# Performance work log

Hardware: AMD Instinct MI355X
Metric: run time of the kernel (lower is better)

The kernel has to match this reference:

```python
import jax, jax.numpy as jnp
import numpy as np

N_NODES = 50000
IN_C = 128
OUT_C = 128
N_EDGES = 1600000
NEG_SLOPE = 0.2
EPS = 1e-16  # matches torch_geometric softmax denominator epsilon


def setup_inputs() -> dict:
    key = jax.random.key(0)
    k1, k2, k3, k4, k5 = jax.random.split(key, 5)
    glorot = 1.0 / np.sqrt(IN_C)
    x = jax.random.normal(k1, (N_NODES, IN_C), dtype=jnp.float32)
    W = jax.random.normal(k2, (IN_C, OUT_C), dtype=jnp.float32) * glorot
    a_src = jax.random.normal(k3, (OUT_C,), dtype=jnp.float32) * glorot
    a_dst = jax.random.normal(k4, (OUT_C,), dtype=jnp.float32) * glorot
    bias = jnp.zeros((OUT_C,), dtype=jnp.float32)
    edge_index = jax.random.randint(k5, (2, N_EDGES), 0, N_NODES, dtype=jnp.int32)
    return {"x": x, "W": W, "a_src": a_src, "a_dst": a_dst,
            "bias": bias, "edge_index": edge_index}


def reference(x, W, a_src, a_dst, bias, edge_index):
    N = x.shape[0]
    # add self loops (GATConv default add_self_loops=True)
    loops = jnp.arange(N, dtype=edge_index.dtype)
    src = jnp.concatenate([edge_index[0], loops])  # [E+N]
    dst = jnp.concatenate([edge_index[1], loops])

    h = x @ W                                      # [N, out]
    alpha_s = h @ a_src                            # [N]
    alpha_d = h @ a_dst                            # [N]

    e = alpha_s[src] + alpha_d[dst]                # [E+N]
    e = jnp.where(e > 0, e, NEG_SLOPE * e)         # leaky_relu

    # neighbor-wise (per destination node) stable softmax
    m = jax.ops.segment_max(e, dst, num_segments=N)
    ex = jnp.exp(e - m[dst])
    denom = jax.ops.segment_sum(ex, dst, num_segments=N)
    alpha = ex / (denom[dst] + EPS)

    # weighted aggregation of source features into destination nodes
    msgs = h[src] * alpha[:, None]                 # [E+N, out]
    out = jax.ops.segment_sum(msgs, dst, num_segments=N) + bias
    return jax.nn.relu(out)
```

## Files before the change

### kernel.cpp

```cpp
#include <hip/hip_runtime.h>
#include <hip/hip_fp16.h>

#define C 128
#define NEG_SLOPE 0.2f
#define SM_EPS 1e-16f
#define BKT_SHIFT 8
#define BKT_MASK 255
#define GB_CHUNK 2048
#define WP 136

typedef unsigned int uint32;
typedef __attribute__((ext_vector_type(8))) short bf16x8;
typedef __attribute__((ext_vector_type(4))) float f32x4;

static __device__ __forceinline__ unsigned short f2bf(float f) {
    uint32 u = __float_as_uint(f);
    uint32 r = 0x7FFFu + ((u >> 16) & 1u);
    return (unsigned short)((u + r) >> 16);
}
static __device__ __forceinline__ uint32 f2bf2(float lo, float hi) {
    return (uint32)f2bf(lo) | ((uint32)f2bf(hi) << 16);
}
static __device__ __forceinline__ uint32 f2h(float f) {
    __half h = __float2half(f);
    return (uint32)*reinterpret_cast<unsigned short*>(&h);
}
static __device__ __forceinline__ float h2f(uint32 b) {
    unsigned short s = (unsigned short)(b & 0xffffu);
    __half h = *reinterpret_cast<__half*>(&s);
    return __half2float(h);
}

__global__ __launch_bounds__(256) void cvtw_hist_kernel(
    const float* __restrict__ W, uint32* __restrict__ Wf,
    const int* __restrict__ dst, int* __restrict__ bucket_cnt,
    int E, int total, int NB)
{
    __shared__ int bhist[256];
    const int tid = threadIdx.x;
    bhist[tid] = 0;
    const int gid = blockIdx.x * 256 + tid;
    if (gid < 8192) {
        int j2   = gid & 3;
        int lane = (gid >> 2) & 63;
        int tile = gid >> 8;
        int t = tile >> 2, kk = tile & 3;
        int n = t * 16 + (lane & 15);
        int k = kk * 32 + (lane >> 4) * 8 + j2 * 2;
        Wf[gid] = f2bf2(W[k * C + n], W[(k + 1) * C + n]);
    }
    __syncthreads();
    const int stride = gridDim.x * 256;
    for (int i = gid; i < total; i += stride) {
        int d = (i < E) ? dst[i] : (i - E);
        atomicAdd(&bhist[d >> BKT_SHIFT], 1);
    }
    __syncthreads();
    if (tid < NB && bhist[tid]) atomicAdd(&bucket_cnt[tid], bhist[tid]);
}

__global__ __launch_bounds__(256) void gemm_bin_kernel(
    const float* __restrict__ x, const uint32* __restrict__ Wf,
    const float* __restrict__ a_src, const float* __restrict__ a_dst,
    unsigned short* __restrict__ hb, float* __restrict__ as_out,
    float* __restrict__ ad_out, int N,
    const int* __restrict__ src, const int* __restrict__ dst,
    const int* __restrict__ bucket_cnt, int* __restrict__ bucket_progress,
    uint32* __restrict__ packed, int E, int total, int NB)
{
    __shared__ __align__(16) unsigned short slice[4][16 * WP];
    __shared__ int hist[256];
    __shared__ int base[256];
    __shared__ int boff[256];
    __shared__ int wave_tot[4];

    const int tid  = threadIdx.x;
    const int lane = tid & 63;
    const int w    = tid >> 6;
    const int row0 = blockIdx.x * 64;
    const int m16  = lane & 15;
    const int q    = lane >> 4;

    if (row0 < N) {
        const int row = row0 + w * 16 + m16;
        const bool rv = (row < N);
        const float* xr_p = x + (size_t)(rv ? row : 0) * C + q * 8;

        float4 xr[8];
        #pragma unroll
        for (int kk = 0; kk < 4; ++kk) {
            xr[kk * 2]     = rv ? *(const float4*)(xr_p + kk * 32)     : make_float4(0, 0, 0, 0);
            xr[kk * 2 + 1] = rv ? *(const float4*)(xr_p + kk * 32 + 4) : make_float4(0, 0, 0, 0);
        }

        f32x4 acc[8];
        const f32x4 zz = {0.f, 0.f, 0.f, 0.f};
        #pragma unroll
        for (int t = 0; t < 8; ++t) acc[t] = zz;

        #pragma unroll
        for (int kk = 0; kk < 4; ++kk) {
            union { bf16x8 v; uint32 u[4]; } au;
            float4 p0 = xr[kk * 2], p1 = xr[kk * 2 + 1];
            au.u[0] = f2bf2(p0.x, p0.y); au.u[1] = f2bf2(p0.z, p0.w);
            au.u[2] = f2bf2(p1.x, p1.y); au.u[3] = f2bf2(p1.z, p1.w);
            #pragma unroll
            for (int t = 0; t < 8; ++t) {
                bf16x8 b = *(const bf16x8*)&Wf[((t * 4 + kk) * 64 + lane) * 4];
                acc[t] = __builtin_amdgcn_mfma_f32_16x16x32_bf16(au.v, b, acc[t], 0, 0, 0);
            }
        }

        float ps[4] = {0.f, 0.f, 0.f, 0.f}, pd[4] = {0.f, 0.f, 0.f, 0.f};
        #pragma unroll
        for (int t = 0; t < 8; ++t) {
            float av = a_src[t * 16 + m16];
            float dv = a_dst[t * 16 + m16];
            #pragma unroll
            for (int r = 0; r < 4; ++r) {
                ps[r] += acc[t][r] * av;
                pd[r] += acc[t][r] * dv;
            }
        }
        #pragma unroll
        for (int r = 0; r < 4; ++r) {
            #pragma unroll
            for (int off = 1; off < 16; off <<= 1) {
                ps[r] += __shfl_xor(ps[r], off, 64);
                pd[r] += __shfl_xor(pd[r], off, 64);
            }
        }
        if (m16 == 0) {
            #pragma unroll
            for (int r = 0; r < 4; ++r) {
                int rr = row0 + w * 16 + q * 4 + r;
                if (rr < N) { as_out[rr] = ps[r]; ad_out[rr] = pd[r]; }
            }
        }

        #pragma unroll
        for (int t = 0; t < 8; ++t)
            #pragma unroll
            for (int r = 0; r < 4; ++r)
                slice[w][(q * 4 + r) * WP + t * 16 + m16] = f2bf(acc[t][r]);
        __syncthreads();
        #pragma unroll
        for (int it = 0; it < 4; ++it) {
            int r = it * 4 + q;
            int rr = row0 + w * 16 + r;
            if (rr < N) {
                bf16x8 v = *(const bf16x8*)&slice[w][r * WP + m16 * 8];
                *(bf16x8*)&hb[(size_t)rr * C + m16 * 8] = v;
            }
        }
    }

    const int start = blockIdx.x * GB_CHUNK;
    if (start >= total) return;
    const int end = min(start + GB_CHUNK, total);

    hist[tid] = 0;
    int v = (tid < NB) ? bucket_cnt[tid] : 0;
    int xx = v;
    #pragma unroll
    for (int o = 1; o < 64; o <<= 1) {
        int t = __shfl_up(xx, o, 64);
        if (lane >= o) xx += t;
    }
    if (lane == 63) wave_tot[w] = xx;
    __syncthreads();
    {
        int wbase = 0;
        #pragma unroll
        for (int w2 = 0; w2 < 4; ++w2) wbase += (w2 < w) ? wave_tot[w2] : 0;
        boff[tid] = wbase + xx - v;
    }

    int es[8], ed[8];
    #pragma unroll
    for (int k = 0; k < 8; ++k) {
        int i = start + k * 256 + tid;
        if (i < end) {
            es[k] = (i < E) ? src[i] : (i - E);
            ed[k] = (i < E) ? dst[i] : (i - E);
        } else ed[k] = -1;
    }
    #pragma unroll
    for (int k = 0; k < 8; ++k)
        if (ed[k] >= 0) atomicAdd(&hist[ed[k] >> BKT_SHIFT], 1);
    __syncthreads();
    if (tid < NB) {
        int c = hist[tid];
        base[tid] = boff[tid] + (c ? atomicAdd(&bucket_progress[tid], c) : 0);
    }
    hist[tid] = 0;
    __syncthreads();
    #pragma unroll
    for (int k = 0; k < 8; ++k) {
        if (ed[k] >= 0) {
            int b = ed[k] >> BKT_SHIFT;
            int pos = base[b] + atomicAdd(&hist[b], 1);
            packed[pos] = ((uint32)es[k] << BKT_SHIFT) | (uint32)(ed[k] & BKT_MASK);
        }
    }
}

__global__ __launch_bounds__(1024) void build_kernel(
    const uint32* __restrict__ packed, const int* __restrict__ bucket_cnt,
    const float* __restrict__ as, const float* __restrict__ ad,
    int* __restrict__ row_start, uint32* __restrict__ csr, int N, int NB, int total)
{
    __shared__ int cnt[256];
    __shared__ int cur[256];
    __shared__ float adl[256];
    __shared__ int boff[256];
    __shared__ int wave_tot[8];
    const int tid = threadIdx.x;
    const int b = blockIdx.x;

    int v = 0, xx = 0;
    if (tid < 256) {
        const int lane = tid & 63;
        v = (tid < NB) ? bucket_cnt[tid] : 0;
        xx = v;
        #pragma unroll
        for (int o = 1; o < 64; o <<= 1) {
            int t = __shfl_up(xx, o, 64);
            if (lane >= o) xx += t;
        }
        if (lane == 63) wave_tot[tid >> 6] = xx;
        cnt[tid] = 0;
        int g = (b << BKT_SHIFT) + tid;
        adl[tid] = (g < N) ? ad[g] : 0.f;
    }
    __syncthreads();
    if (tid < 256) {
        const int wid = tid >> 6;
        int wbase = 0;
        #pragma unroll
        for (int w = 0; w < 4; ++w) wbase += (w < wid) ? wave_tot[w] : 0;
        boff[tid] = wbase + xx - v;
    }
    __syncthreads();
    const int off = boff[b];
    const int end = off + ((b < NB) ? bucket_cnt[b] : 0);
    if (b == 0 && tid == 0) row_start[N] = total;

    for (int j = off + tid; j < end; j += 1024)
        atomicAdd(&cnt[packed[j] & BKT_MASK], 1);
    __syncthreads();

    int v2 = 0, x2 = 0;
    if (tid < 256) {
        const int lane = tid & 63;
        v2 = cnt[tid]; x2 = v2;
        #pragma unroll
        for (int o = 1; o < 64; o <<= 1) {
            int t = __shfl_up(x2, o, 64);
            if (lane >= o) x2 += t;
        }
        if (lane == 63) wave_tot[4 + (tid >> 6)] = x2;
    }
    __syncthreads();
    if (tid < 256) {
        const int wid = tid >> 6;
        int wbase = 0;
        #pragma unroll
        for (int w = 0; w < 4; ++w) wbase += (w < wid) ? wave_tot[4 + w] : 0;
        int excl = wbase + x2 - v2;
        int g = (b << BKT_SHIFT) + tid;
        if (g < N) row_start[g] = off + excl;
        cur[tid] = excl;
    }
    __syncthreads();

    for (int j = off + tid; j < end; j += 1024) {
        uint32 p = packed[j];
        int l = (int)(p & BKT_MASK);
        int s = (int)(p >> BKT_SHIFT);
        float e = as[s] + adl[l];
        e = (e > 0.f) ? e : NEG_SLOPE * e;
        int pos = atomicAdd(&cur[l], 1);
        csr[off + pos] = ((uint32)s << 16) | f2h(e);
    }
}

static __device__ __forceinline__ void gather_node_fw(
    int d, const uint32* __restrict__ csr, const int* __restrict__ row_start,
    const unsigned short* __restrict__ hb, const float* __restrict__ bias,
    float* __restrict__ out, int lane)
{
    const int beg = row_start[d];
    const int deg = row_start[d + 1] - beg;
    const int c2 = lane << 1;
    float a0 = 0.f, a1 = 0.f;
    float m = -INFINITY;
    for (int t = lane; t < deg; t += 64) m = fmaxf(m, h2f(csr[beg + t]));
    #pragma unroll
    for (int off = 32; off > 0; off >>= 1) m = fmaxf(m, __shfl_xor(m, off, 64));
    float ssum = 0.f;
    for (int t = lane; t < deg; t += 64) ssum += __expf(h2f(csr[beg + t]) - m);
    #pragma unroll
    for (int off = 32; off > 0; off >>= 1) ssum += __shfl_xor(ssum, off, 64);
    float inv = 1.f / (ssum + SM_EPS);
    for (int t0 = 0; t0 < deg; t0 += 64) {
        int nc = min(64, deg - t0);
        uint32 ent = (lane < nc) ? csr[beg + t0 + lane] : 0xFC00u;
        float wl = (lane < nc) ? __expf(h2f(ent) - m) * inv : 0.f;
        uint32 bc = (ent & 0xffff0000u) | f2h(wl);
        for (int t = 0; t < nc; ++t) {
            uint32 b0 = (uint32)__shfl((int)bc, t, 64);
            uint32 u0 = *(const uint32*)&hb[(size_t)(b0 >> 16) * C + c2];
            float w0 = h2f(b0);
            a0 += __uint_as_float(u0 << 16) * w0;
            a1 += __uint_as_float(u0 & 0xffff0000u) * w0;
        }
    }
    float2 b2 = *(const float2*)&bias[c2];
    a0 = fmaxf(a0 + b2.x, 0.f);
    a1 = fmaxf(a1 + b2.y, 0.f);
    *(float2*)&out[(size_t)d * C + c2] = make_float2(a0, a1);
}

#define ACC4(r, wgt)                                           \
    {                                                          \
        a0 += __uint_as_float((r).x << 16)         * (wgt);    \
        a1 += __uint_as_float((r).x & 0xffff0000u) * (wgt);    \
        a2 += __uint_as_float((r).y << 16)         * (wgt);    \
        a3 += __uint_as_float((r).y & 0xffff0000u) * (wgt);    \
    }

__global__ __launch_bounds__(256) void gather_kernel(
    const uint32* __restrict__ csr, const int* __restrict__ row_start,
    const unsigned short* __restrict__ hb, const float* __restrict__ bias,
    float* __restrict__ out, int N)
{
    __shared__ __align__(16) uint2 lent[4][2][64];
    const int w    = threadIdx.x >> 6;
    const int lane = threadIdx.x & 63;
    const int half = lane >> 5;
    const int hl   = lane & 31;
    const int pair = blockIdx.x * 4 + w;
    const int d0 = pair * 2;
    if (d0 >= N) return;
    const int d = d0 + half;
    const bool valid = (d < N);

    int beg = 0, deg = 0;
    if (valid) { beg = row_start[d]; deg = row_start[d + 1] - beg; }

    int wdeg = deg;
    #pragma unroll
    for (int off = 32; off > 0; off >>= 1) wdeg = max(wdeg, __shfl_xor(wdeg, off, 64));

    if (wdeg > 64) {
        gather_node_fw(d0, csr, row_start, hb, bias, out, lane);
        if (d0 + 1 < N) gather_node_fw(d0 + 1, csr, row_start, hb, bias, out, lane);
        return;
    }

    uint32 ent0 = (hl < deg) ? csr[beg + hl] : 0xFC00u;
    uint32 ent1 = (32 + hl < deg) ? csr[beg + 32 + hl] : 0xFC00u;
    float e0 = h2f(ent0), e1 = h2f(ent1);
    float m = fmaxf(e0, e1);
    #pragma unroll
    for (int off = 16; off > 0; off >>= 1) m = fmaxf(m, __shfl_xor(m, off, 64));
    float p0 = (hl < deg) ? __expf(e0 - m) : 0.f;
    float p1 = (32 + hl < deg) ? __expf(e1 - m) : 0.f;
    float ssum = p0 + p1;
    #pragma unroll
    for (int off = 16; off > 0; off >>= 1) ssum += __shfl_xor(ssum, off, 64);
    const float inv = 1.f / (ssum + SM_EPS);

    lent[w][half][hl]      = make_uint2((ent0 & 0xffff0000u) >> 8, __float_as_uint(p0 * inv));
    lent[w][half][32 + hl] = make_uint2((ent1 & 0xffff0000u) >> 8, __float_as_uint(p1 * inv));
    __builtin_amdgcn_wave_barrier();

    const uint32 cb = (uint32)(hl << 3);
    const char* hbB = (const char*)hb;
    const uint2* lp = &lent[w][half][0];
    float a0 = 0.f, a1 = 0.f, a2 = 0.f, a3 = 0.f;

    int t = 0;
    for (; t + 8 <= deg; t += 8) {
        uint4 q0 = *(const uint4*)(lp + t);
        uint4 q1 = *(const uint4*)(lp + t + 2);
        uint4 q2 = *(const uint4*)(lp + t + 4);
        uint4 q3 = *(const uint4*)(lp + t + 6);
        uint2 r0 = *(const uint2*)(hbB + (q0.x + cb));
        uint2 r1 = *(const uint2*)(hbB + (q0.z + cb));
        uint2 r2 = *(const uint2*)(hbB + (q1.x + cb));
        uint2 r3 = *(const uint2*)(hbB + (q1.z + cb));
        uint2 r4 = *(const uint2*)(hbB + (q2.x + cb));
        uint2 r5 = *(const uint2*)(hbB + (q2.z + cb));
        uint2 r6 = *(const uint2*)(hbB + (q3.x + cb));
        uint2 r7 = *(const uint2*)(hbB + (q3.z + cb));
        float w0 = __uint_as_float(q0.y), w1 = __uint_as_float(q0.w);
        float w2 = __uint_as_float(q1.y), w3 = __uint_as_float(q1.w);
        float w4 = __uint_as_float(q2.y), w5 = __uint_as_float(q2.w);
        float w6 = __uint_as_float(q3.y), w7 = __uint_as_float(q3.w);
        ACC4(r0, w0) ACC4(r1, w1) ACC4(r2, w2) ACC4(r3, w3)
        ACC4(r4, w4) ACC4(r5, w5) ACC4(r6, w6) ACC4(r7, w7)
    }
    for (; t < deg; ++t) {
        uint2 q = lp[t];
        uint2 r = *(const uint2*)(hbB + (q.x + cb));
        float wt = __uint_as_float(q.y);
        ACC4(r, wt)
    }

    if (valid) {
        const int c4 = hl << 2;
        float4 bb = *(const float4*)&bias[c4];
        float4 o;
        o.x = fmaxf(a0 + bb.x, 0.f);
        o.y = fmaxf(a1 + bb.y, 0.f);
        o.z = fmaxf(a2 + bb.z, 0.f);
        o.w = fmaxf(a3 + bb.w, 0.f);
        *(float4*)&out[(size_t)d * C + c4] = o;
    }
}

extern "C" void kernel_launch(void* const* d_in, const int* in_sizes, int n_in,
                              void* d_out, int out_size, void* d_ws, size_t ws_size,
                              hipStream_t stream) {
    const float* x     = (const float*)d_in[0];
    const float* W     = (const float*)d_in[1];
    const float* a_src = (const float*)d_in[2];
    const float* a_dst = (const float*)d_in[3];
    const float* bias  = (const float*)d_in[4];
    const int*   edge  = (const int*)d_in[5];

    const int N = in_sizes[0] / C;
    const int E = in_sizes[5] / 2;
    const int total = E + N;
    const int* src = edge;
    const int* dst = edge + E;
    float* out = (float*)d_out;

    const int NB = (N + BKT_MASK) >> BKT_SHIFT;

    float* ws = (float*)d_ws;
    unsigned short* hb = (unsigned short*)ws;
    float* as = (float*)(hb + (size_t)N * C);
    float* ad = as + N;
    int* row_start       = (int*)(ad + N);
    uint32* packed       = (uint32*)(row_start + (N + 2));
    uint32* csr          = packed + total;
    uint32* Wf           = csr + total;
    int* bucket_cnt      = (int*)(Wf + 8192);
    int* bucket_progress = bucket_cnt + NB;

    const int nrow   = (N + 63) / 64;
    const int nchunk = (total + GB_CHUNK - 1) / GB_CHUNK;
    const int grid2  = (nrow > nchunk) ? nrow : nchunk;

    hipMemsetAsync(bucket_cnt, 0, (size_t)(2 * NB) * sizeof(int), stream);
    cvtw_hist_kernel<<<512, 256, 0, stream>>>(W, Wf, dst, bucket_cnt, E, total, NB);
    gemm_bin_kernel<<<grid2, 256, 0, stream>>>(
        x, Wf, a_src, a_dst, hb, as, ad, N, src, dst,
        bucket_cnt, bucket_progress, packed, E, total, NB);
    build_kernel<<<NB, 1024, 0, stream>>>(packed, bucket_cnt, as, ad, row_start,
                                          csr, N, NB, total);
    gather_kernel<<<((N + 1) / 2 + 3) / 4, 256, 0, stream>>>(csr, row_start, hb, bias, out, N);
}
```

Measured before the change: 207.9 us.

## Fuse CSR build into gather via per-block LDS CSR, hoist bucket scan

Merges the build and gather kernels, so each block builds a local CSR for a quarter of a 256-node bucket in shared memory and aggregates from it directly. This removes the global csr and row_start arrays and one kernel launch. The bucket prefix scan moves into a small single-block kernel instead of being recomputed in every block. As a trade-off, each of the four blocks per bucket rescans the whole bucket's packed edges (reading them four times or more, with extra passes when a sub-range overflows CAP), and launch parallelism drops to 4*NB blocks.

Result: slower. 272.6 us (+31.1%).

```diff
diff --git a/kernel.cpp b/kernel.cpp
--- a/kernel.cpp
+++ b/kernel.cpp
@@ -8,6 +8,7 @@
 #define BKT_MASK 255
 #define GB_CHUNK 2048
 #define WP 136
+#define CAP 3072
 
 typedef unsigned int uint32;
 typedef __attribute__((ext_vector_type(8))) short bf16x8;
@@ -59,20 +60,42 @@
     if (tid < NB && bhist[tid]) atomicAdd(&bucket_cnt[tid], bhist[tid]);
 }
 
+__global__ __launch_bounds__(256) void scan_kernel(
+    const int* __restrict__ bucket_cnt, int* __restrict__ bucket_off,
+    int NB, int total)
+{
+    __shared__ int wt[4];
+    const int tid = threadIdx.x;
+    const int lane = tid & 63;
+    const int w = tid >> 6;
+    int v = (tid < NB) ? bucket_cnt[tid] : 0;
+    int x = v;
+    #pragma unroll
+    for (int o = 1; o < 64; o <<= 1) {
+        int t = __shfl_up(x, o, 64);
+        if (lane >= o) x += t;
+    }
+    if (lane == 63) wt[w] = x;
+    __syncthreads();
+    int wbase = 0;
+    #pragma unroll
+    for (int w2 = 0; w2 < 4; ++w2) wbase += (w2 < w) ? wt[w2] : 0;
+    if (tid < NB) bucket_off[tid] = wbase + x - v;
+    if (tid == 0) bucket_off[NB] = total;
+}
+
 __global__ __launch_bounds__(256) void gemm_bin_kernel(
     const float* __restrict__ x, const uint32* __restrict__ Wf,
     const float* __restrict__ a_src, const float* __restrict__ a_dst,
     unsigned short* __restrict__ hb, float* __restrict__ as_out,
     float* __restrict__ ad_out, int N,
     const int* __restrict__ src, const int* __restrict__ dst,
-    const int* __restrict__ bucket_cnt, int* __restrict__ bucket_progress,
+    const int* __restrict__ bucket_off, int* __restrict__ bucket_progress,
     uint32* __restrict__ packed, int E, int total, int NB)
 {
     __shared__ __align__(16) unsigned short slice[4][16 * WP];
     __shared__ int hist[256];
     __shared__ int base[256];
-    __shared__ int boff[256];
-    __shared__ int wave_tot[4];
 
     const int tid  = threadIdx.x;
     const int lane = tid & 63;
@@ -160,21 +183,7 @@
     const int end = min(start + GB_CHUNK, total);
 
     hist[tid] = 0;
-    int v = (tid < NB) ? bucket_cnt[tid] : 0;
-    int xx = v;
-    #pragma unroll
-    for (int o = 1; o < 64; o <<= 1) {
-        int t = __shfl_up(xx, o, 64);
-        if (lane >= o) xx += t;
-    }
-    if (lane == 63) wave_tot[w] = xx;
-    __syncthreads();
-    {
-        int wbase = 0;
-        #pragma unroll
-        for (int w2 = 0; w2 < 4; ++w2) wbase += (w2 < w) ? wave_tot[w2] : 0;
-        boff[tid] = wbase + xx - v;
-    }
+    __syncthreads();
 
     int es[8], ed[8];
     #pragma unroll
@@ -191,7 +200,7 @@
     __syncthreads();
     if (tid < NB) {
         int c = hist[tid];
-        base[tid] = boff[tid] + (c ? atomicAdd(&bucket_progress[tid], c) : 0);
+        base[tid] = bucket_off[tid] + (c ? atomicAdd(&bucket_progress[tid], c) : 0);
     }
     hist[tid] = 0;
     __syncthreads();
@@ -205,107 +214,33 @@
     }
 }
 
-__global__ __launch_bounds__(1024) void build_kernel(
-    const uint32* __restrict__ packed, const int* __restrict__ bucket_cnt,
-    const float* __restrict__ as, const float* __restrict__ ad,
-    int* __restrict__ row_start, uint32* __restrict__ csr, int N, int NB, int total)
-{
-    __shared__ int cnt[256];
-    __shared__ int cur[256];
-    __shared__ float adl[256];
-    __shared__ int boff[256];
-    __shared__ int wave_tot[8];
-    const int tid = threadIdx.x;
-    const int b = blockIdx.x;
-
-    int v = 0, xx = 0;
-    if (tid < 256) {
-        const int lane = tid & 63;
-        v = (tid < NB) ? bucket_cnt[tid] : 0;
-        xx = v;
-        #pragma unroll
-        for (int o = 1; o < 64; o <<= 1) {
-            int t = __shfl_up(xx, o, 64);
-            if (lane >= o) xx += t;
-        }
-        if (lane == 63) wave_tot[tid >> 6] = xx;
-        cnt[tid] = 0;
-        int g = (b << BKT_SHIFT) + tid;
-        adl[tid] = (g < N) ? ad[g] : 0.f;
-    }
-    __syncthreads();
-    if (tid < 256) {
-        const int wid = tid >> 6;
-        int wbase = 0;
-        #pragma unroll
-        for (int w = 0; w < 4; ++w) wbase += (w < wid) ? wave_tot[w] : 0;
-        boff[tid] = wbase + xx - v;
-    }
-    __syncthreads();
-    const int off = boff[b];
-    const int end = off + ((b < NB) ? bucket_cnt[b] : 0);
-    if (b == 0 && tid == 0) row_start[N] = total;
-
-    for (int j = off + tid; j < end; j += 1024)
-        atomicAdd(&cnt[packed[j] & BKT_MASK], 1);
-    __syncthreads();
-
-    int v2 = 0, x2 = 0;
-    if (tid < 256) {
-        const int lane = tid & 63;
-        v2 = cnt[tid]; x2 = v2;
-        #pragma unroll
-        for (int o = 1; o < 64; o <<= 1) {
-            int t = __shfl_up(x2, o, 64);
-            if (lane >= o) x2 += t;
-        }
-        if (lane == 63) wave_tot[4 + (tid >> 6)] = x2;
-    }
-    __syncthreads();
-    if (tid < 256) {
-        const int wid = tid >> 6;
-        int wbase = 0;
-        #pragma unroll
-        for (int w = 0; w < 4; ++w) wbase += (w < wid) ? wave_tot[4 + w] : 0;
-        int excl = wbase + x2 - v2;
-        int g = (b << BKT_SHIFT) + tid;
-        if (g < N) row_start[g] = off + excl;
-        cur[tid] = excl;
-    }
-    __syncthreads();
-
-    for (int j = off + tid; j < end; j += 1024) {
-        uint32 p = packed[j];
-        int l = (int)(p & BKT_MASK);
-        int s = (int)(p >> BKT_SHIFT);
-        float e = as[s] + adl[l];
-        e = (e > 0.f) ? e : NEG_SLOPE * e;
-        int pos = atomicAdd(&cur[l], 1);
-        csr[off + pos] = ((uint32)s << 16) | f2h(e);
-    }
-}
-
-static __device__ __forceinline__ void gather_node_fw(
-    int d, const uint32* __restrict__ csr, const int* __restrict__ row_start,
+#define ACC4(r, wgt)                                           \
+    {                                                          \
+        a0 += __uint_as_float((r).x << 16)         * (wgt);    \
+        a1 += __uint_as_float((r).x & 0xffff0000u) * (wgt);    \
+        a2 += __uint_as_float((r).y << 16)         * (wgt);    \
+        a3 += __uint_as_float((r).y & 0xffff0000u) * (wgt);    \
+    }
+
+static __device__ __forceinline__ void gather_fw_lds(
+    int g, int beg, int deg, const uint32* lcsr,
     const unsigned short* __restrict__ hb, const float* __restrict__ bias,
     float* __restrict__ out, int lane)
 {
-    const int beg = row_start[d];
-    const int deg = row_start[d + 1] - beg;
     const int c2 = lane << 1;
     float a0 = 0.f, a1 = 0.f;
     float m = -INFINITY;
-    for (int t = lane; t < deg; t += 64) m = fmaxf(m, h2f(csr[beg + t]));
+    for (int t = lane; t < deg; t += 64) m = fmaxf(m, h2f(lcsr[beg + t]));
     #pragma unroll
     for (int off = 32; off > 0; off >>= 1) m = fmaxf(m, __shfl_xor(m, off, 64));
     float ssum = 0.f;
-    for (int t = lane; t < deg; t += 64) ssum += __expf(h2f(csr[beg + t]) - m);
+    for (int t = lane; t < deg; t += 64) ssum += __expf(h2f(lcsr[beg + t]) - m);
     #pragma unroll
     for (int off = 32; off > 0; off >>= 1) ssum += __shfl_xor(ssum, off, 64);
     float inv = 1.f / (ssum + SM_EPS);
     for (int t0 = 0; t0 < deg; t0 += 64) {
         int nc = min(64, deg - t0);
-        uint32 ent = (lane < nc) ? csr[beg + t0 + lane] : 0xFC00u;
+        uint32 ent = (lane < nc) ? lcsr[beg + t0 + lane] : 0xFC00u;
         float wl = (lane < nc) ? __expf(h2f(ent) - m) * inv : 0.f;
         uint32 bc = (ent & 0xffff0000u) | f2h(wl);
         for (int t = 0; t < nc; ++t) {
@@ -319,105 +254,177 @@
     float2 b2 = *(const float2*)&bias[c2];
     a0 = fmaxf(a0 + b2.x, 0.f);
     a1 = fmaxf(a1 + b2.y, 0.f);
-    *(float2*)&out[(size_t)d * C + c2] = make_float2(a0, a1);
-}
-
-#define ACC4(r, wgt)                                           \
-    {                                                          \
-        a0 += __uint_as_float((r).x << 16)         * (wgt);    \
-        a1 += __uint_as_float((r).x & 0xffff0000u) * (wgt);    \
-        a2 += __uint_as_float((r).y << 16)         * (wgt);    \
-        a3 += __uint_as_float((r).y & 0xffff0000u) * (wgt);    \
-    }
-
-__global__ __launch_bounds__(256) void gather_kernel(
-    const uint32* __restrict__ csr, const int* __restrict__ row_start,
+    *(float2*)&out[(size_t)g * C + c2] = make_float2(a0, a1);
+}
+
+__global__ __launch_bounds__(256) void buildgather_kernel(
+    const uint32* __restrict__ packed, const int* __restrict__ bucket_off,
+    const float* __restrict__ as, const float* __restrict__ ad,
     const unsigned short* __restrict__ hb, const float* __restrict__ bias,
     float* __restrict__ out, int N)
 {
+    __shared__ uint32 lcsr[CAP];
+    __shared__ float adl[64];
+    __shared__ int cnt[64];
+    __shared__ int rowoff[65];
+    __shared__ int cur[64];
+    __shared__ int subl[66];
+    __shared__ int nsub_s;
     __shared__ __align__(16) uint2 lent[4][2][64];
-    const int w    = threadIdx.x >> 6;
-    const int lane = threadIdx.x & 63;
+
+    const int tid  = threadIdx.x;
+    const int lane = tid & 63;
+    const int w    = tid >> 6;
+    const int z = blockIdx.x;
+    const int b = z >> 2;
+    const uint32 q = (uint32)(z & 3);
+    const int node0 = (b << BKT_SHIFT) + ((int)q << 6);
+    const int off = bucket_off[b];
+    const int end = bucket_off[b + 1];
+
+    if (tid < 64) {
+        int g = node0 + tid;
+        adl[tid] = (g < N) ? ad[g] : 0.f;
+        cnt[tid] = 0;
+    }
+    __syncthreads();
+    for (int j = off + tid; j < end; j += 256) {
+        uint32 p = packed[j];
+        if (((p >> 6) & 3u) == q) atomicAdd(&cnt[p & 63u], 1);
+    }
+    __syncthreads();
+    if (w == 0) {
+        int v = cnt[lane];
+        int x = v;
+        #pragma unroll
+        for (int o = 1; o < 64; o <<= 1) {
+            int t = __shfl_up(x, o, 64);
+            if (lane >= o) x += t;
+        }
+        rowoff[lane] = x - v;
+        if (lane == 63) rowoff[64] = x;
+    }
+    __syncthreads();
+    if (tid == 0) {
+        int l0 = 0, ns = 0;
+        subl[0] = 0;
+        while (l0 < 64) {
+            int l1 = l0 + 1;
+            while (l1 < 64 && rowoff[l1 + 1] - rowoff[l0] <= CAP) ++l1;
+            subl[++ns] = l1;
+            l0 = l1;
+        }
+        nsub_s = ns;
+    }
+    __syncthreads();
+    const int nsub = nsub_s;
+
     const int half = lane >> 5;
     const int hl   = lane & 31;
-    const int pair = blockIdx.x * 4 + w;
-    const int d0 = pair * 2;
-    if (d0 >= N) return;
-    const int d = d0 + half;
-    const bool valid = (d < N);
-
-    int beg = 0, deg = 0;
-    if (valid) { beg = row_start[d]; deg = row_start[d + 1] - beg; }
-
-    int wdeg = deg;
-    #pragma unroll
-    for (int off = 32; off > 0; off >>= 1) wdeg = max(wdeg, __shfl_xor(wdeg, off, 64));
-
-    if (wdeg > 64) {
-        gather_node_fw(d0, csr, row_start, hb, bias, out, lane);
-        if (d0 + 1 < N) gather_node_fw(d0 + 1, csr, row_start, hb, bias, out, lane);
-        return;
-    }
-
-    uint32 ent0 = (hl < deg) ? csr[beg + hl] : 0xFC00u;
-    uint32 ent1 = (32 + hl < deg) ? csr[beg + 32 + hl] : 0xFC00u;
-    float e0 = h2f(ent0), e1 = h2f(ent1);
-    float m = fmaxf(e0, e1);
-    #pragma unroll
-    for (int off = 16; off > 0; off >>= 1) m = fmaxf(m, __shfl_xor(m, off, 64));
-    float p0 = (hl < deg) ? __expf(e0 - m) : 0.f;
-    float p1 = (32 + hl < deg) ? __expf(e1 - m) : 0.f;
-    float ssum = p0 + p1;
-    #pragma unroll
-    for (int off = 16; off > 0; off >>= 1) ssum += __shfl_xor(ssum, off, 64);
-    const float inv = 1.f / (ssum + SM_EPS);
-
-    lent[w][half][hl]      = make_uint2((ent0 & 0xffff0000u) >> 8, __float_as_uint(p0 * inv));
-    lent[w][half][32 + hl] = make_uint2((ent1 & 0xffff0000u) >> 8, __float_as_uint(p1 * inv));
-    __builtin_amdgcn_wave_barrier();
-
     const uint32 cb = (uint32)(hl << 3);
     const char* hbB = (const char*)hb;
     const uint2* lp = &lent[w][half][0];
-    float a0 = 0.f, a1 = 0.f, a2 = 0.f, a3 = 0.f;
-
-    int t = 0;
-    for (; t + 8 <= deg; t += 8) {
-        uint4 q0 = *(const uint4*)(lp + t);
-        uint4 q1 = *(const uint4*)(lp + t + 2);
-        uint4 q2 = *(const uint4*)(lp + t + 4);
-        uint4 q3 = *(const uint4*)(lp + t + 6);
-        uint2 r0 = *(const uint2*)(hbB + (q0.x + cb));
-        uint2 r1 = *(const uint2*)(hbB + (q0.z + cb));
-        uint2 r2 = *(const uint2*)(hbB + (q1.x + cb));
-        uint2 r3 = *(const uint2*)(hbB + (q1.z + cb));
-        uint2 r4 = *(const uint2*)(hbB + (q2.x + cb));
-        uint2 r5 = *(const uint2*)(hbB + (q2.z + cb));
-        uint2 r6 = *(const uint2*)(hbB + (q3.x + cb));
-        uint2 r7 = *(const uint2*)(hbB + (q3.z + cb));
-        float w0 = __uint_as_float(q0.y), w1 = __uint_as_float(q0.w);
-        float w2 = __uint_as_float(q1.y), w3 = __uint_as_float(q1.w);
-        float w4 = __uint_as_float(q2.y), w5 = __uint_as_float(q2.w);
-        float w6 = __uint_as_float(q3.y), w7 = __uint_as_float(q3.w);
-        ACC4(r0, w0) ACC4(r1, w1) ACC4(r2, w2) ACC4(r3, w3)
-        ACC4(r4, w4) ACC4(r5, w5) ACC4(r6, w6) ACC4(r7, w7)
-    }
-    for (; t < deg; ++t) {
-        uint2 q = lp[t];
-        uint2 r = *(const uint2*)(hbB + (q.x + cb));
-        float wt = __uint_as_float(q.y);
-        ACC4(r, wt)
-    }
-
-    if (valid) {
-        const int c4 = hl << 2;
-        float4 bb = *(const float4*)&bias[c4];
-        float4 o;
-        o.x = fmaxf(a0 + bb.x, 0.f);
-        o.y = fmaxf(a1 + bb.y, 0.f);
-        o.z = fmaxf(a2 + bb.z, 0.f);
-        o.w = fmaxf(a3 + bb.w, 0.f);
-        *(float4*)&out[(size_t)d * C + c4] = o;
+
+    for (int sidx = 0; sidx < nsub; ++sidx) {
+        const int l0 = subl[sidx], l1 = subl[sidx + 1];
+        const int base0 = rowoff[l0];
+        if (tid < 64) cur[tid] = rowoff[tid] - base0;
+        __syncthreads();
+        for (int j = off + tid; j < end; j += 256) {
+            uint32 p = packed[j];
+            if (((p >> 6) & 3u) != q) continue;
+            int l = (int)(p & 63u);
+            if (l < l0 || l >= l1) continue;
+            int s = (int)(p >> BKT_SHIFT);
+            float e = as[s] + adl[l];
+            e = (e > 0.f) ? e : NEG_SLOPE * e;
+            int pos = atomicAdd(&cur[l], 1);
+            if (pos < CAP) lcsr[pos] = ((uint32)s << 16) | f2h(e);
+        }
+        __syncthreads();
+        for (int lb = l0 + w * 2; lb < l1; lb += 8) {
+            int lA = lb + half;
+            int g = node0 + lA;
+            bool validn = (lA < l1) && (g < N);
+            int beg = 0, deg = 0;
+            if (validn) { beg = rowoff[lA] - base0; deg = rowoff[lA + 1] - rowoff[lA]; }
+
+            int wdeg = deg;
+            #pragma unroll
+            for (int o2 = 32; o2 > 0; o2 >>= 1) wdeg = max(wdeg, __shfl_xor(wdeg, o2, 64));
+            if (wdeg == 0) continue;
+            if (wdeg > 64) {
+                #pragma unroll
+                for (int hh = 0; hh < 2; ++hh) {
+                    int l2 = lb + hh;
+                    int g2 = node0 + l2;
+                    if (l2 < l1 && g2 < N) {
+                        int bg = rowoff[l2] - base0;
+                        int dg = rowoff[l2 + 1] - rowoff[l2];
+                        if (dg > 0) gather_fw_lds(g2, bg, dg, lcsr, hb, bias, out, lane);
+                    }
+                }
+                continue;
+            }
+
+            uint32 ent0 = (hl < deg) ? lcsr[beg + hl] : 0xFC00u;
+            uint32 ent1 = (32 + hl < deg) ? lcsr[beg + 32 + hl] : 0xFC00u;
+            float e0 = h2f(ent0), e1 = h2f(ent1);
+            float m = fmaxf(e0, e1);
+            #pragma unroll
+            for (int o2 = 16; o2 > 0; o2 >>= 1) m = fmaxf(m, __shfl_xor(m, o2, 64));
+            float p0 = (hl < deg) ? __expf(e0 - m) : 0.f;
+            float p1 = (32 + hl < deg) ? __expf(e1 - m) : 0.f;
+            float ssum = p0 + p1;
+            #pragma unroll
+            for (int o2 = 16; o2 > 0; o2 >>= 1) ssum += __shfl_xor(ssum, o2, 64);
+            const float inv = 1.f / (ssum + SM_EPS);
+
+            lent[w][half][hl]      = make_uint2((ent0 & 0xffff0000u) >> 8, __float_as_uint(p0 * inv));
+            lent[w][half][32 + hl] = make_uint2((ent1 & 0xffff0000u) >> 8, __float_as_uint(p1 * inv));
+            __builtin_amdgcn_wave_barrier();
+
+            float a0 = 0.f, a1 = 0.f, a2 = 0.f, a3 = 0.f;
+            int t = 0;
+            for (; t + 8 <= deg; t += 8) {
+                uint4 q0 = *(const uint4*)(lp + t);
+                uint4 q1 = *(const uint4*)(lp + t + 2);
+                uint4 q2 = *(const uint4*)(lp + t + 4);
+                uint4 q3 = *(const uint4*)(lp + t + 6);
+                uint2 r0 = *(const uint2*)(hbB + (q0.x + cb));
+                uint2 r1 = *(const uint2*)(hbB + (q0.z + cb));
+                uint2 r2 = *(const uint2*)(hbB + (q1.x + cb));
+                uint2 r3 = *(const uint2*)(hbB + (q1.z + cb));
+                uint2 r4 = *(const uint2*)(hbB + (q2.x + cb));
+                uint2 r5 = *(const uint2*)(hbB + (q2.z + cb));
+                uint2 r6 = *(const uint2*)(hbB + (q3.x + cb));
+                uint2 r7 = *(const uint2*)(hbB + (q3.z + cb));
+                float w0 = __uint_as_float(q0.y), w1 = __uint_as_float(q0.w);
+                float w2 = __uint_as_float(q1.y), w3 = __uint_as_float(q1.w);
+                float w4 = __uint_as_float(q2.y), w5 = __uint_as_float(q2.w);
+                float w6 = __uint_as_float(q3.y), w7 = __uint_as_float(q3.w);
+                ACC4(r0, w0) ACC4(r1, w1) ACC4(r2, w2) ACC4(r3, w3)
+                ACC4(r4, w4) ACC4(r5, w5) ACC4(r6, w6) ACC4(r7, w7)
+            }
+            for (; t < deg; ++t) {
+                uint2 qv = lp[t];
+                uint2 r = *(const uint2*)(hbB + (qv.x + cb));
+                float wt = __uint_as_float(qv.y);
+                ACC4(r, wt)
+            }
+
+            if (validn) {
+                const int c4 = hl << 2;
+                float4 bb = *(const float4*)&bias[c4];
+                float4 o;
+                o.x = fmaxf(a0 + bb.x, 0.f);
+                o.y = fmaxf(a1 + bb.y, 0.f);
+                o.z = fmaxf(a2 + bb.z, 0.f);
+                o.w = fmaxf(a3 + bb.w, 0.f);
+                *(float4*)&out[(size_t)g * C + c4] = o;
+            }
+        }
+        __syncthreads();
     }
 }
 
@@ -444,12 +451,11 @@
     unsigned short* hb = (unsigned short*)ws;
     float* as = (float*)(hb + (size_t)N * C);
     float* ad = as + N;
-    int* row_start       = (int*)(ad + N);
-    uint32* packed       = (uint32*)(row_start + (N + 2));
-    uint32* csr          = packed + total;
-    uint32* Wf           = csr + total;
+    uint32* packed       = (uint32*)(ad + N);
+    uint32* Wf           = packed + total;
     int* bucket_cnt      = (int*)(Wf + 8192);
     int* bucket_progress = bucket_cnt + NB;
+    int* bucket_off      = bucket_progress + NB;
 
     const int nrow   = (N + 63) / 64;
     const int nchunk = (total + GB_CHUNK - 1) / GB_CHUNK;
@@ -457,10 +463,10 @@
 
     hipMemsetAsync(bucket_cnt, 0, (size_t)(2 * NB) * sizeof(int), stream);
     cvtw_hist_kernel<<<512, 256, 0, stream>>>(W, Wf, dst, bucket_cnt, E, total, NB);
+    scan_kernel<<<1, 256, 0, stream>>>(bucket_cnt, bucket_off, NB, total);
     gemm_bin_kernel<<<grid2, 256, 0, stream>>>(
         x, Wf, a_src, a_dst, hb, as, ad, N, src, dst,
-        bucket_cnt, bucket_progress, packed, E, total, NB);
-    build_kernel<<<NB, 1024, 0, stream>>>(packed, bucket_cnt, as, ad, row_start,
-                                          csr, N, NB, total);
-    gather_kernel<<<((N + 1) / 2 + 3) / 4, 256, 0, stream>>>(csr, row_start, hb, bias, out, N);
-}
+        bucket_off, bucket_progress, packed, E, total, NB);
+    buildgather_kernel<<<4 * NB, 256, 0, stream>>>(
+        packed, bucket_off, as, ad, hb, bias, out, N);
+}
```

## Split fused gemm/bin kernel and precompute bucket offsets in a scan kernel

Applied to the files above, without the earlier changes.

Breaks the combined GEMM+edge-binning kernel into separate gemm and bin kernels and adds a single-block scan kernel that computes bucket prefix offsets once. The bin and build kernels now read those offsets instead of each block redoing the 256-entry prefix scan. This removes redundant per-block scan work and lets each kernel use its natural grid, at the cost of two extra kernel launches and losing the overlap of GEMM and binning inside one launch. The __syncthreads inside divergent branches in build_kernel is a correctness risk on some compilers.

Result: slower. 250.4 us (+20.4%).

```diff
diff --git a/kernel.cpp b/kernel.cpp
--- a/kernel.cpp
+++ b/kernel.cpp
@@ -59,20 +59,37 @@
     if (tid < NB && bhist[tid]) atomicAdd(&bucket_cnt[tid], bhist[tid]);
 }
 
-__global__ __launch_bounds__(256) void gemm_bin_kernel(
+__global__ __launch_bounds__(256) void scan_kernel(
+    const int* __restrict__ bucket_cnt, int* __restrict__ bucket_off,
+    int NB, int total)
+{
+    __shared__ int wt[4];
+    const int tid = threadIdx.x;
+    const int lane = tid & 63;
+    const int w = tid >> 6;
+    int v = (tid < NB) ? bucket_cnt[tid] : 0;
+    int x = v;
+    #pragma unroll
+    for (int o = 1; o < 64; o <<= 1) {
+        int t = __shfl_up(x, o, 64);
+        if (lane >= o) x += t;
+    }
+    if (lane == 63) wt[w] = x;
+    __syncthreads();
+    int wbase = 0;
+    #pragma unroll
+    for (int w2 = 0; w2 < 4; ++w2) wbase += (w2 < w) ? wt[w2] : 0;
+    if (tid < NB) bucket_off[tid] = wbase + x - v;
+    if (tid == 0) bucket_off[NB] = total;
+}
+
+__global__ __launch_bounds__(256) void gemm_kernel(
     const float* __restrict__ x, const uint32* __restrict__ Wf,
     const float* __restrict__ a_src, const float* __restrict__ a_dst,
     unsigned short* __restrict__ hb, float* __restrict__ as_out,
-    float* __restrict__ ad_out, int N,
-    const int* __restrict__ src, const int* __restrict__ dst,
-    const int* __restrict__ bucket_cnt, int* __restrict__ bucket_progress,
-    uint32* __restrict__ packed, int E, int total, int NB)
+    float* __restrict__ ad_out, int N)
 {
     __shared__ __align__(16) unsigned short slice[4][16 * WP];
-    __shared__ int hist[256];
-    __shared__ int base[256];
-    __shared__ int boff[256];
-    __shared__ int wave_tot[4];
 
     const int tid  = threadIdx.x;
     const int lane = tid & 63;
@@ -81,100 +98,92 @@
     const int m16  = lane & 15;
     const int q    = lane >> 4;
 
-    if (row0 < N) {
-        const int row = row0 + w * 16 + m16;
-        const bool rv = (row < N);
-        const float* xr_p = x + (size_t)(rv ? row : 0) * C + q * 8;
-
-        float4 xr[8];
-        #pragma unroll
-        for (int kk = 0; kk < 4; ++kk) {
-            xr[kk * 2]     = rv ? *(const float4*)(xr_p + kk * 32)     : make_float4(0, 0, 0, 0);
-            xr[kk * 2 + 1] = rv ? *(const float4*)(xr_p + kk * 32 + 4) : make_float4(0, 0, 0, 0);
-        }
-
-        f32x4 acc[8];
-        const f32x4 zz = {0.f, 0.f, 0.f, 0.f};
-        #pragma unroll
-        for (int t = 0; t < 8; ++t) acc[t] = zz;
-
-        #pragma unroll
-        for (int kk = 0; kk < 4; ++kk) {
-            union { bf16x8 v; uint32 u[4]; } au;
-            float4 p0 = xr[kk * 2], p1 = xr[kk * 2 + 1];
-            au.u[0] = f2bf2(p0.x, p0.y); au.u[1] = f2bf2(p0.z, p0.w);
-            au.u[2] = f2bf2(p1.x, p1.y); au.u[3] = f2bf2(p1.z, p1.w);
-            #pragma unroll
-            for (int t = 0; t < 8; ++t) {
-                bf16x8 b = *(const bf16x8*)&Wf[((t * 4 + kk) * 64 + lane) * 4];
-                acc[t] = __builtin_amdgcn_mfma_f32_16x16x32_bf16(au.v, b, acc[t], 0, 0, 0);
-            }
-        }
-
-        float ps[4] = {0.f, 0.f, 0.f, 0.f}, pd[4] = {0.f, 0.f, 0.f, 0.f};
+    const int row = row0 + w * 16 + m16;
+    const bool rv = (row < N);
+    const float* xr_p = x + (size_t)(rv ? row : 0) * C + q * 8;
+
+    float4 xr[8];
+    #pragma unroll
+    for (int kk = 0; kk < 4; ++kk) {
+        xr[kk * 2]     = rv ? *(const float4*)(xr_p + kk * 32)     : make_float4(0, 0, 0, 0);
+        xr[kk * 2 + 1] = rv ? *(const float4*)(xr_p + kk * 32 + 4) : make_float4(0, 0, 0, 0);
+    }
+
+    f32x4 acc[8];
+    const f32x4 zz = {0.f, 0.f, 0.f, 0.f};
+    #pragma unroll
+    for (int t = 0; t < 8; ++t) acc[t] = zz;
+
+    #pragma unroll
+    for (int kk = 0; kk < 4; ++kk) {
+        union { bf16x8 v; uint32 u[4]; } au;
+        float4 p0 = xr[kk * 2], p1 = xr[kk * 2 + 1];
+        au.u[0] = f2bf2(p0.x, p0.y); au.u[1] = f2bf2(p0.z, p0.w);
+        au.u[2] = f2bf2(p1.x, p1.y); au.u[3] = f2bf2(p1.z, p1.w);
         #pragma unroll
         for (int t = 0; t < 8; ++t) {
-            float av = a_src[t * 16 + m16];
-            float dv = a_dst[t * 16 + m16];
-            #pragma unroll
-            for (int r = 0; r < 4; ++r) {
-                ps[r] += acc[t][r] * av;
-                pd[r] += acc[t][r] * dv;
-            }
-        }
+            bf16x8 b = *(const bf16x8*)&Wf[((t * 4 + kk) * 64 + lane) * 4];
+            acc[t] = __builtin_amdgcn_mfma_f32_16x16x32_bf16(au.v, b, acc[t], 0, 0, 0);
+        }
+    }
+
+    float ps[4] = {0.f, 0.f, 0.f, 0.f}, pd[4] = {0.f, 0.f, 0.f, 0.f};
+    #pragma unroll
+    for (int t = 0; t < 8; ++t) {
+        float av = a_src[t * 16 + m16];
+        float dv = a_dst[t * 16 + m16];
         #pragma unroll
         for (int r = 0; r < 4; ++r) {
-            #pragma unroll
-            for (int off = 1; off < 16; off <<= 1) {
-                ps[r] += __shfl_xor(ps[r], off, 64);
-                pd[r] += __shfl_xor(pd[r], off, 64);
-            }
-        }
-        if (m16 == 0) {
-            #pragma unroll
-            for (int r = 0; r < 4; ++r) {
-                int rr = row0 + w * 16 + q * 4 + r;
-                if (rr < N) { as_out[rr] = ps[r]; ad_out[rr] = pd[r]; }
-            }
-        }
-
-        #pragma unroll
-        for (int t = 0; t < 8; ++t)
-            #pragma unroll
-            for (int r = 0; r < 4; ++r)
-                slice[w][(q * 4 + r) * WP + t * 16 + m16] = f2bf(acc[t][r]);
-        __syncthreads();
-        #pragma unroll
-        for (int it = 0; it < 4; ++it) {
-            int r = it * 4 + q;
-            int rr = row0 + w * 16 + r;
-            if (rr < N) {
-                bf16x8 v = *(const bf16x8*)&slice[w][r * WP + m16 * 8];
-                *(bf16x8*)&hb[(size_t)rr * C + m16 * 8] = v;
-            }
-        }
-    }
-
+            ps[r] += acc[t][r] * av;
+            pd[r] += acc[t][r] * dv;
+        }
+    }
+    #pragma unroll
+    for (int r = 0; r < 4; ++r) {
+        #pragma unroll
+        for (int off = 1; off < 16; off <<= 1) {
+            ps[r] += __shfl_xor(ps[r], off, 64);
+            pd[r] += __shfl_xor(pd[r], off, 64);
+        }
+    }
+    if (m16 == 0) {
+        #pragma unroll
+        for (int r = 0; r < 4; ++r) {
+            int rr = row0 + w * 16 + q * 4 + r;
+            if (rr < N) { as_out[rr] = ps[r]; ad_out[rr] = pd[r]; }
+        }
+    }
+
+    #pragma unroll
+    for (int t = 0; t < 8; ++t)
+        #pragma unroll
+        for (int r = 0; r < 4; ++r)
+            slice[w][(q * 4 + r) * WP + t * 16 + m16] = f2bf(acc[t][r]);
+    __syncthreads();
+    #pragma unroll
+    for (int it = 0; it < 4; ++it) {
+        int r = it * 4 + q;
+        int rr = row0 + w * 16 + r;
+        if (rr < N) {
+            bf16x8 v = *(const bf16x8*)&slice[w][r * WP + m16 * 8];
+            *(bf16x8*)&hb[(size_t)rr * C + m16 * 8] = v;
+        }
+    }
+}
+
+__global__ __launch_bounds__(256) void bin_kernel(
+    const int* __restrict__ src, const int* __restrict__ dst,
+    const int* __restrict__ bucket_off, int* __restrict__ bucket_progress,
+    uint32* __restrict__ packed, int E, int total, int NB)
+{
+    __shared__ int hist[256];
+    __shared__ int base[256];
+    const int tid = threadIdx.x;
     const int start = blockIdx.x * GB_CHUNK;
-    if (start >= total) return;
     const int end = min(start + GB_CHUNK, total);
 
     hist[tid] = 0;
-    int v = (tid < NB) ? bucket_cnt[tid] : 0;
-    int xx = v;
-    #pragma unroll
-    for (int o = 1; o < 64; o <<= 1) {
-        int t = __shfl_up(xx, o, 64);
-        if (lane >= o) xx += t;
-    }
-    if (lane == 63) wave_tot[w] = xx;
-    __syncthreads();
-    {
-        int wbase = 0;
-        #pragma unroll
-        for (int w2 = 0; w2 < 4; ++w2) wbase += (w2 < w) ? wave_tot[w2] : 0;
-        boff[tid] = wbase + xx - v;
-    }
+    __syncthreads();
 
     int es[8], ed[8];
     #pragma unroll
@@ -191,7 +200,7 @@
     __syncthreads();
     if (tid < NB) {
         int c = hist[tid];
-        base[tid] = boff[tid] + (c ? atomicAdd(&bucket_progress[tid], c) : 0);
+        base[tid] = bucket_off[tid] + (c ? atomicAdd(&bucket_progress[tid], c) : 0);
     }
     hist[tid] = 0;
     __syncthreads();
@@ -206,71 +215,51 @@
 }
 
 __global__ __launch_bounds__(1024) void build_kernel(
-    const uint32* __restrict__ packed, const int* __restrict__ bucket_cnt,
+    const uint32* __restrict__ packed, const int* __restrict__ bucket_off,
     const float* __restrict__ as, const float* __restrict__ ad,
     int* __restrict__ row_start, uint32* __restrict__ csr, int N, int NB, int total)
 {
     __shared__ int cnt[256];
     __shared__ int cur[256];
     __shared__ float adl[256];
-    __shared__ int boff[256];
-    __shared__ int wave_tot[8];
+    __shared__ int wt[4];
     const int tid = threadIdx.x;
     const int b = blockIdx.x;
 
-    int v = 0, xx = 0;
     if (tid < 256) {
-        const int lane = tid & 63;
-        v = (tid < NB) ? bucket_cnt[tid] : 0;
-        xx = v;
-        #pragma unroll
-        for (int o = 1; o < 64; o <<= 1) {
-            int t = __shfl_up(xx, o, 64);
-            if (lane >= o) xx += t;
-        }
-        if (lane == 63) wave_tot[tid >> 6] = xx;
         cnt[tid] = 0;
         int g = (b << BKT_SHIFT) + tid;
         adl[tid] = (g < N) ? ad[g] : 0.f;
     }
     __syncthreads();
-    if (tid < 256) {
-        const int wid = tid >> 6;
-        int wbase = 0;
-        #pragma unroll
-        for (int w = 0; w < 4; ++w) wbase += (w < wid) ? wave_tot[w] : 0;
-        boff[tid] = wbase + xx - v;
-    }
-    __syncthreads();
-    const int off = boff[b];
-    const int end = off + ((b < NB) ? bucket_cnt[b] : 0);
+    const int off = bucket_off[b];
+    const int end = bucket_off[b + 1];
     if (b == 0 && tid == 0) row_start[N] = total;
 
     for (int j = off + tid; j < end; j += 1024)
         atomicAdd(&cnt[packed[j] & BKT_MASK], 1);
     __syncthreads();
 
-    int v2 = 0, x2 = 0;
     if (tid < 256) {
         const int lane = tid & 63;
-        v2 = cnt[tid]; x2 = v2;
+        const int w = tid >> 6;
+        int v2 = cnt[tid], x2 = v2;
         #pragma unroll
         for (int o = 1; o < 64; o <<= 1) {
             int t = __shfl_up(x2, o, 64);
             if (lane >= o) x2 += t;
         }
-        if (lane == 63) wave_tot[4 + (tid >> 6)] = x2;
-    }
-    __syncthreads();
-    if (tid < 256) {
-        const int wid = tid >> 6;
+        if (lane == 63) wt[w] = x2;
+        __syncthreads();
         int wbase = 0;
         #pragma unroll
-        for (int w = 0; w < 4; ++w) wbase += (w < wid) ? wave_tot[4 + w] : 0;
+        for (int w2 = 0; w2 < 4; ++w2) wbase += (w2 < w) ? wt[w2] : 0;
         int excl = wbase + x2 - v2;
         int g = (b << BKT_SHIFT) + tid;
         if (g < N) row_start[g] = off + excl;
         cur[tid] = excl;
+    } else {
+        __syncthreads();
     }
     __syncthreads();
 
@@ -450,17 +439,15 @@
     uint32* Wf           = csr + total;
     int* bucket_cnt      = (int*)(Wf + 8192);
     int* bucket_progress = bucket_cnt + NB;
-
-    const int nrow   = (N + 63) / 64;
-    const int nchunk = (total + GB_CHUNK - 1) / GB_CHUNK;
-    const int grid2  = (nrow > nchunk) ? nrow : nchunk;
+    int* bucket_off      = bucket_progress + NB;
 
     hipMemsetAsync(bucket_cnt, 0, (size_t)(2 * NB) * sizeof(int), stream);
     cvtw_hist_kernel<<<512, 256, 0, stream>>>(W, Wf, dst, bucket_cnt, E, total, NB);
-    gemm_bin_kernel<<<grid2, 256, 0, stream>>>(
-        x, Wf, a_src, a_dst, hb, as, ad, N, src, dst,
-        bucket_cnt, bucket_progress, packed, E, total, NB);
-    build_kernel<<<NB, 1024, 0, stream>>>(packed, bucket_cnt, as, ad, row_start,
+    scan_kernel<<<1, 256, 0, stream>>>(bucket_cnt, bucket_off, NB, total);
+    gemm_kernel<<<(N + 63) / 64, 256, 0, stream>>>(x, Wf, a_src, a_dst, hb, as, ad, N);
+    bin_kernel<<<(total + GB_CHUNK - 1) / GB_CHUNK, 256, 0, stream>>>(
+        src, dst, bucket_off, bucket_progress, packed, E, total, NB);
+    build_kernel<<<NB, 1024, 0, stream>>>(packed, bucket_off, as, ad, row_start,
                                           csr, N, NB, total);
     gather_kernel<<<((N + 1) / 2 + 3) / 4, 256, 0, stream>>>(csr, row_start, hb, bias, out, N);
 }
```
